# Kernel optimization log

Measured on AMD Instinct MI355X. Metric: run time of the kernel, lower is better.

The kernel has to match this reference:

```python
import jax, jax.numpy as jnp
import numpy as np

B, S, D, H, E, K = 4, 512, 1024, 16, 4, 2
HD = D // H
LN_EPS = 1e-5


def setup_inputs() -> dict:
    key = jax.random.key(0)
    ks = jax.random.split(key, 16)
    def w(k, shape, fan_in):
        return jax.random.normal(k, shape, jnp.float32) / np.float32(np.sqrt(fan_in))
    return {
        "x": jax.random.normal(ks[0], (B, S, D), jnp.float32),
        # stacked per-expert attention params [E, D, D] / [E, D]
        "Wq": w(ks[1], (E, D, D), D), "bq": jnp.zeros((E, D), jnp.float32),
        "Wk": w(ks[2], (E, D, D), D), "bk": jnp.zeros((E, D), jnp.float32),
        "Wv": w(ks[3], (E, D, D), D), "bv": jnp.zeros((E, D), jnp.float32),
        "Wo": w(ks[4], (E, D, D), D), "bo": jnp.zeros((E, D), jnp.float32),
        # router: Linear(D->D/2), LayerNorm, relu, Linear(D/2->E)
        "Wr1": w(ks[5], (D, D // 2), D), "br1": jnp.zeros((D // 2,), jnp.float32),
        "ln_g": jnp.ones((D // 2,), jnp.float32), "ln_b": jnp.zeros((D // 2,), jnp.float32),
        "Wr2": w(ks[6], (D // 2, E), D // 2), "br2": jnp.zeros((E,), jnp.float32),
    }


def _moe_attention(x, Wq, bq, Wk, bk, Wv, bv, Wo, bo, Wr1, br1, ln_g, ln_b, Wr2, br2):
    # ---- router ----
    h = x @ Wr1 + br1                                        # [B,S,D/2]
    mu = jnp.mean(h, axis=-1, keepdims=True)
    var = jnp.var(h, axis=-1, keepdims=True)
    h = (h - mu) * jax.lax.rsqrt(var + LN_EPS) * ln_g + ln_b
    h = jax.nn.relu(h)
    logits = h @ Wr2 + br2                                   # [B,S,E]
    probs = jax.nn.softmax(logits, axis=-1)
    top_p, top_i = jax.lax.top_k(probs, K)                   # [B,S,K]
    # scatter-add of top-k probs into dense expert mask [B,S,E]
    emask = jnp.sum(jax.nn.one_hot(top_i, E, dtype=x.dtype) * top_p[..., None], axis=2)

    # ---- dense per-expert attention (naive: every expert on every token) ----
    def heads(t):  # [E,B,S,D] -> [E,B,H,S,HD]
        return t.reshape(E, B, S, H, HD).transpose(0, 1, 3, 2, 4)

    q = heads(jnp.einsum('bsd,edf->ebsf', x, Wq) + bq[:, None, None, :])
    k = heads(jnp.einsum('bsd,edf->ebsf', x, Wk) + bk[:, None, None, :])
    v = heads(jnp.einsum('bsd,edf->ebsf', x, Wv) + bv[:, None, None, :])

    scores = jnp.einsum('ebhqd,ebhkd->ebhqk', q, k) / np.float32(np.sqrt(HD))
    attn = jax.nn.softmax(scores, axis=-1)                   # [E,B,H,S,S]
    o = jnp.einsum('ebhqk,ebhkd->ebhqd', attn, v)
    o = o.transpose(0, 1, 3, 2, 4).reshape(E, B, S, D)
    o = jnp.einsum('ebsd,edf->ebsf', o, Wo) + bo[:, None, None, :]  # [E,B,S,D]

    # ---- masked combine ----
    return jnp.einsum('ebsd,bse->bsd', o, emask)


def reference(x, Wq, bq, Wk, bk, Wv, bv, Wo, bo, Wr1, br1, ln_g, ln_b, Wr2, br2):
    return _moe_attention(x, Wq, bq, Wk, bk, Wv, bv, Wo, bo,
                          Wr1, br1, ln_g, ln_b, Wr2, br2)
```

## Files before the change

kernel.cpp:

```cpp
#include <hip/hip_runtime.h>
#include <hip/hip_bf16.h>
#include <math.h>

#define B_   4
#define S_   512
#define D_   1024
#define H_   16
#define E_   4
#define HD_  64
#define D2_  512
#define NTOK (B_*S_)

#define TDE ((size_t)NTOK * D_)
#define WWE ((size_t)D_ * D_)
#define ND2 ((size_t)NTOK * D2_)

typedef unsigned short ushort;
typedef short shortv8 __attribute__((ext_vector_type(8)));
typedef ushort ushortv4 __attribute__((ext_vector_type(4)));
typedef _Float16 halfv8 __attribute__((ext_vector_type(8)));
typedef _Float16 halfv4 __attribute__((ext_vector_type(4)));
typedef float floatv4 __attribute__((ext_vector_type(4)));

__device__ __forceinline__ ushort f2bf(float f) {
    union { __hip_bfloat16 b; ushort u; } cv;
    cv.b = __float2bfloat16(f);
    return cv.u;
}
__device__ __forceinline__ float bf2f(ushort u) {
    union { ushort u; __hip_bfloat16 b; } cv;
    cv.u = u;
    return __bfloat162float(cv.b);
}
__device__ __forceinline__ void gload16(const void* g, void* l) {
    __builtin_amdgcn_global_load_lds(
        (const __attribute__((address_space(1))) unsigned int*)g,
        (__attribute__((address_space(3))) unsigned int*)l, 16, 0, 0);
}

__device__ __forceinline__ void gemm_core_bf(
    const ushort* __restrict__ A0, const ushort* __restrict__ A1,
    const ushort* __restrict__ B0, const ushort* __restrict__ B1,
    int K, int klen, int brow, int bcol, ushort* lds, floatv4 acc[4][4])
{
    const int tid  = threadIdx.x;
    const int wave = tid >> 6, lane = tid & 63;
    const int wm = wave >> 1, wn = wave & 1;
    const int lr = lane & 15, lc = lane >> 4;

    const ushort* gsrc[4] = {A0, A1, B0, B1};
    size_t goff[4][2];
    int    loff[4][2];
#pragma unroll
    for (int t = 0; t < 4; t++) {
#pragma unroll
        for (int s = 0; s < 2; s++) {
            int p = s * 256 + tid;
            int m = p >> 2;
            int c = (p & 3) ^ ((m >> 1) & 3);
            int r = (t < 2) ? (brow + m) : (bcol + m);
            goff[t][s] = (size_t)r * K + c * 8;
            loff[t][s] = t * 4096 + p * 8;
        }
    }

    int aoff[4], boff[4];
#pragma unroll
    for (int i = 0; i < 4; i++) {
        int ra = wm * 64 + i * 16 + lr;
        aoff[i] = ra * 32 + ((lc ^ ((ra >> 1) & 3)) * 8);
        int rb2 = wn * 64 + i * 16 + lr;
        boff[i] = rb2 * 32 + ((lc ^ ((rb2 >> 1) & 3)) * 8);
    }

#define STAGEB_(buf, kk) \
    _Pragma("unroll") for (int t = 0; t < 4; t++) \
    _Pragma("unroll") for (int s = 0; s < 2; s++) \
        gload16(gsrc[t] + goff[t][s] + (kk), lds + (buf) * 16384 + loff[t][s]);

    STAGEB_(0, 0)

    int cur = 0;
    for (int k0 = 0; k0 < klen; k0 += 32, cur ^= 1) {
        if (k0 + 32 < klen) {
            STAGEB_(cur ^ 1, k0 + 32)
            asm volatile("s_waitcnt vmcnt(8)" ::: "memory");
        } else {
            asm volatile("s_waitcnt vmcnt(0)" ::: "memory");
        }
        __builtin_amdgcn_s_barrier();
        __builtin_amdgcn_sched_barrier(0);

        const ushort* L = lds + cur * 16384;
        shortv8 ah[4], al[4], bh[4], bl[4];
#pragma unroll
        for (int i = 0; i < 4; i++) {
            ah[i] = *(const shortv8*)(L +         aoff[i]);
            al[i] = *(const shortv8*)(L +  4096 + aoff[i]);
            bh[i] = *(const shortv8*)(L +  8192 + boff[i]);
            bl[i] = *(const shortv8*)(L + 12288 + boff[i]);
        }
#pragma unroll
        for (int mi = 0; mi < 4; mi++)
#pragma unroll
            for (int nj = 0; nj < 4; nj++) {
                acc[mi][nj] = __builtin_amdgcn_mfma_f32_16x16x32_bf16(ah[mi], bh[nj], acc[mi][nj], 0, 0, 0);
                acc[mi][nj] = __builtin_amdgcn_mfma_f32_16x16x32_bf16(ah[mi], bl[nj], acc[mi][nj], 0, 0, 0);
                acc[mi][nj] = __builtin_amdgcn_mfma_f32_16x16x32_bf16(al[mi], bh[nj], acc[mi][nj], 0, 0, 0);
            }

        asm volatile("s_waitcnt lgkmcnt(0)" ::: "memory");
        __builtin_amdgcn_sched_barrier(0);
        __builtin_amdgcn_s_barrier();
    }
#undef STAGEB_
}

template<bool GATHER>
__device__ __forceinline__ void gemm_core_h1(
    const _Float16* __restrict__ A0, const _Float16* __restrict__ B0,
    const int* __restrict__ arow,
    int K, int klen, int brow, int bcol, _Float16* lds, floatv4 acc[4][4])
{
    const int tid  = threadIdx.x;
    const int wave = tid >> 6, lane = tid & 63;
    const int wm = wave >> 1, wn = wave & 1;
    const int lr = lane & 15, lc = lane >> 4;

    const _Float16* gsrc[2] = {A0, B0};
    size_t goff[2][2];
    int    loff[2][2];
#pragma unroll
    for (int t = 0; t < 2; t++) {
#pragma unroll
        for (int s = 0; s < 2; s++) {
            int p = s * 256 + tid;
            int m = p >> 2;
            int c = (p & 3) ^ ((m >> 1) & 3);
            int r;
            if (t == 0) r = GATHER ? (arow[m] & 0x7FFFFFFF) : (brow + m);
            else        r = bcol + m;
            goff[t][s] = (size_t)r * K + c * 8;
            loff[t][s] = t * 4096 + p * 8;
        }
    }

    int aoff[4], boff[4];
#pragma unroll
    for (int i = 0; i < 4; i++) {
        int ra = wm * 64 + i * 16 + lr;
        aoff[i] = ra * 32 + ((lc ^ ((ra >> 1) & 3)) * 8);
        int rb2 = wn * 64 + i * 16 + lr;
        boff[i] = rb2 * 32 + ((lc ^ ((rb2 >> 1) & 3)) * 8);
    }

#define STAGEH_(buf, kk) \
    _Pragma("unroll") for (int t = 0; t < 2; t++) \
    _Pragma("unroll") for (int s = 0; s < 2; s++) \
        gload16(gsrc[t] + goff[t][s] + (kk), lds + (buf) * 8192 + loff[t][s]);

    STAGEH_(0, 0)

    int cur = 0;
    for (int k0 = 0; k0 < klen; k0 += 32, cur ^= 1) {
        if (k0 + 32 < klen) {
            STAGEH_(cur ^ 1, k0 + 32)
            asm volatile("s_waitcnt vmcnt(4)" ::: "memory");
        } else {
            asm volatile("s_waitcnt vmcnt(0)" ::: "memory");
        }
        __builtin_amdgcn_s_barrier();
        __builtin_amdgcn_sched_barrier(0);

        const _Float16* L = lds + cur * 8192;
        halfv8 aa[4], bb[4];
#pragma unroll
        for (int i = 0; i < 4; i++) {
            aa[i] = *(const halfv8*)(L +        aoff[i]);
            bb[i] = *(const halfv8*)(L + 4096 + boff[i]);
        }
#pragma unroll
        for (int mi = 0; mi < 4; mi++)
#pragma unroll
            for (int nj = 0; nj < 4; nj++)
                acc[mi][nj] = __builtin_amdgcn_mfma_f32_16x16x32_f16(aa[mi], bb[nj], acc[mi][nj], 0, 0, 0);

        asm volatile("s_waitcnt lgkmcnt(0)" ::: "memory");
        __builtin_amdgcn_sched_barrier(0);
        __builtin_amdgcn_s_barrier();
    }
#undef STAGEH_
}

#define ACC_INIT(acc) \
    _Pragma("unroll") for (int i = 0; i < 4; i++) \
    _Pragma("unroll") for (int j = 0; j < 4; j++) \
    _Pragma("unroll") for (int q = 0; q < 4; q++) acc[i][j][q] = 0.f;

#define EPI_VARS \
    const int lane = threadIdx.x & 63, wave = threadIdx.x >> 6; \
    const int wm = wave >> 1, wn = wave & 1, lr = lane & 15, lc = lane >> 4;

__global__ __launch_bounds__(256, 2) void gemm_router(
    const ushort* __restrict__ xh, const ushort* __restrict__ xl,
    const ushort* __restrict__ wr1h, const ushort* __restrict__ wr1l,
    float* __restrict__ hpart)
{
    __shared__ ushort lds[32768];
    floatv4 acc[4][4];
    ACC_INIT(acc)

    const int lid = blockIdx.x + 4 * (blockIdx.y + 16 * blockIdx.z);
    const int nid = (lid & 7) * 32 + (lid >> 3);
    const int kz = nid >> 6;
    const int rem = nid & 63;
    const int brow = (rem >> 2) * 128, bcol = (rem & 3) * 128;

    const int koff = kz * 256;
    gemm_core_bf(xh + koff, xl + koff, wr1h + koff, wr1l + koff,
                 D_, 256, brow, bcol, lds, acc);

    float* C = hpart + (size_t)kz * ND2;
    EPI_VARS
#pragma unroll
    for (int mi = 0; mi < 4; mi++)
#pragma unroll
        for (int nj = 0; nj < 4; nj++)
#pragma unroll
            for (int i = 0; i < 4; i++) {
                int row = brow + wm * 64 + mi * 16 + lc * 4 + i;
                int col = bcol + wn * 64 + nj * 16 + lr;
                C[(size_t)row * D2_ + col] = acc[mi][nj][i];
            }
}

__global__ __launch_bounds__(256, 2) void gemm_proj(
    const _Float16* __restrict__ xf,
    const _Float16* __restrict__ wth,
    const float* __restrict__ bq, const float* __restrict__ bk, const float* __restrict__ bv,
    const int* __restrict__ idx, const int* __restrict__ meta,
    _Float16* __restrict__ qf, _Float16* __restrict__ kf, _Float16* __restrict__ vf)
{
    __shared__ _Float16 lds[16384];
    const int lid = blockIdx.x + 8 * (blockIdx.y + 16 * blockIdx.z);
    const int nid = (lid & 7) * 192 + (lid >> 3);
    const int z = nid >> 7;
    const int rem = nid & 127;
    const int brow = (rem >> 3) * 128, bcol = (rem & 7) * 128;

    if (z < 8) {
        const int slot = z >> 1, m = z & 1;
        const size_t so = (size_t)slot * TDE;
        const _Float16* Bm = wth + (size_t)(slot * 4 + 1 + m) * WWE;
        const float* bias = ((m == 0) ? bk : bv) + (size_t)slot * D_;
        _Float16* Oo = ((m == 0) ? kf : vf) + so;

        floatv4 acc[4][4];
        ACC_INIT(acc)
        gemm_core_h1<false>(xf, Bm, nullptr, D_, D_, brow, bcol, lds, acc);

        EPI_VARS
#pragma unroll
        for (int mi = 0; mi < 4; mi++)
#pragma unroll
            for (int nj = 0; nj < 4; nj++)
#pragma unroll
                for (int i = 0; i < 4; i++) {
                    int row = brow + wm * 64 + mi * 16 + lc * 4 + i;
                    int col = bcol + wn * 64 + nj * 16 + lr;
                    Oo[(size_t)row * D_ + col] = (_Float16)(acc[mi][nj][i] + bias[col]);
                }
    } else {
        const int e = z - 8;
        const int pcnt = meta[32 + e];
        if (brow >= pcnt) return;
        const int* arow = idx + e * 2048 + brow;
        const _Float16* Bm = wth + (size_t)(e * 4 + 0) * WWE;
        const float* bias = bq + (size_t)e * D_;
        const size_t so = (size_t)e * TDE;

        floatv4 acc[4][4];
        ACC_INIT(acc)
        gemm_core_h1<true>(xf, Bm, arow, D_, D_, brow, bcol, lds, acc);

        EPI_VARS
#pragma unroll
        for (int mi = 0; mi < 4; mi++)
#pragma unroll
            for (int nj = 0; nj < 4; nj++)
#pragma unroll
                for (int i = 0; i < 4; i++) {
                    int row = brow + wm * 64 + mi * 16 + lc * 4 + i;
                    int col = bcol + wn * 64 + nj * 16 + lr;
                    qf[so + (size_t)row * D_ + col] =
                        (_Float16)((acc[mi][nj][i] + bias[col]) * 0.125f);
                }
    }
}

__global__ __launch_bounds__(256, 2) void gemm_combine4(
    const _Float16* __restrict__ oh,
    const _Float16* __restrict__ wth,
    const float* __restrict__ bo, const float* __restrict__ emask,
    const int* __restrict__ idx, const int* __restrict__ meta,
    float* __restrict__ out4)
{
    __shared__ _Float16 lds[16384];
    const int lid = blockIdx.x + 8 * (blockIdx.y + 16 * blockIdx.z);
    const int nid = (lid & 7) * 64 + (lid >> 3);
    const int e = nid >> 7;
    const int rem = nid & 127;
    const int brow = (rem >> 3) * 128, bcol = (rem & 7) * 128;

    const int pcnt = meta[32 + e];
    if (brow >= pcnt) return;
    const size_t so = (size_t)e * TDE;
    const _Float16* Bm = wth + (size_t)(e * 4 + 3) * WWE;
    const float* bias = bo + (size_t)e * D_;
    const int* idxe = idx + e * 2048;

    floatv4 acc[4][4];
    ACC_INIT(acc)
    gemm_core_h1<false>(oh + so, Bm, nullptr, D_, D_, brow, bcol, lds, acc);

    float* dst = out4 + so;
    EPI_VARS
#pragma unroll
    for (int mi = 0; mi < 4; mi++)
#pragma unroll
        for (int nj = 0; nj < 4; nj++)
#pragma unroll
            for (int i = 0; i < 4; i++) {
                int srow = brow + wm * 64 + mi * 16 + lc * 4 + i;
                int raw = idxe[srow];
                if (raw >= 0) {
                    float s = emask[(size_t)raw * E_ + e];
                    int col = bcol + wn * 64 + nj * 16 + lr;
                    dst[(size_t)raw * D_ + col] = s * (acc[mi][nj][i] + bias[col]);
                }
            }
}

__global__ __launch_bounds__(256) void reduce_out(
    const float* __restrict__ out4, float* __restrict__ out)
{
    size_t i = (size_t)blockIdx.x * 256 + threadIdx.x;
    const float4* p = (const float4*)out4;
    float4 a = p[i], b = p[i + TDE / 4], c = p[i + 2 * (TDE / 4)], d = p[i + 3 * (TDE / 4)];
    float4 r;
    r.x = a.x + b.x + c.x + d.x;
    r.y = a.y + b.y + c.y + d.y;
    r.z = a.z + b.z + c.z + d.z;
    r.w = a.w + b.w + c.w + d.w;
    ((float4*)out)[i] = r;
}

__global__ __launch_bounds__(256) void build_lists(
    const float* __restrict__ emask, int* __restrict__ idx, int* __restrict__ meta)
{
    const int e = blockIdx.x;
    const int tid = threadIdx.x;
    __shared__ int scan[256];
    __shared__ int runsh;
    if (tid == 0) runsh = 0;
    int* idxe = idx + e * 2048;

    for (int b = 0; b < B_; b++) {
        __syncthreads();
        const int base = runsh;
        int t0 = b * 512 + tid * 2;
        int f0 = (emask[(size_t)t0 * E_ + e] != 0.f) ? 1 : 0;
        int f1 = (emask[(size_t)(t0 + 1) * E_ + e] != 0.f) ? 1 : 0;
        int my = f0 + f1;
        scan[tid] = my;
        __syncthreads();
        for (int off = 1; off < 256; off <<= 1) {
            int v = (tid >= off) ? scan[tid - off] : 0;
            __syncthreads();
            scan[tid] += v;
            __syncthreads();
        }
        int excl = scan[tid] - my;
        int cnt = scan[255];
        if (f0) idxe[base + excl] = t0;
        if (f1) idxe[base + excl + f0] = t0 + 1;
        int plen = (cnt + 63) & ~63;
        for (int i = cnt + tid; i < plen; i += 256)
            idxe[base + i] = (b * 512) | (int)0x80000000;
        if (tid == 0) {
            meta[e * 4 + b] = base;
            meta[16 + e * 4 + b] = plen >> 6;
            runsh = base + plen;
        }
    }
    __syncthreads();
    int total = runsh;
    if (tid == 0) meta[32 + e] = total;
    for (int i = total + tid; i < 2048; i += 256)
        idxe[i] = (int)0x80000000;
}

__global__ __launch_bounds__(256, 2) void attn_all(
    const _Float16* __restrict__ qf_, const _Float16* __restrict__ kf_,
    const _Float16* __restrict__ vf_,
    _Float16* __restrict__ oh_,
    const int* __restrict__ meta)
{
    const int lid = blockIdx.x + 8 * (blockIdx.y + 64 * blockIdx.z);
    const int nid = (lid & 7) * 256 + (lid >> 3);
    const int e = nid >> 9;
    const int rem = nid & 511;
    const int bhid = rem >> 3, qtile = rem & 7;
    const int bb = bhid >> 4, hh = bhid & 15;

    const int ptiles = meta[16 + e * 4 + bb];
    if (qtile >= ptiles) return;
    const int pstart = meta[e * 4 + bb];

    __shared__ _Float16 Kf[4096];
    __shared__ _Float16 Vt[64 * 72];
    __shared__ _Float16 Pw[4][16 * 72];

    const size_t zo = (size_t)e * TDE;
    const int tid = threadIdx.x;
    const int wave = tid >> 6, lane = tid & 63;
    const int lr = lane & 15, lc = lane >> 4;
    const int q0 = pstart + qtile * 64;
    const size_t kvbase = zo + (size_t)bb * S_ * D_ + hh * 64;
    const size_t qobase = zo + hh * 64;

    halfv8 qq[2];
    {
        size_t qoff = qobase + (size_t)(q0 + wave * 16 + lr) * D_ + lc * 8;
        qq[0] = *(const halfv8*)(qf_ + qoff);
        qq[1] = *(const halfv8*)(qf_ + qoff + 32);
    }

    floatv4 ov[4];
    float m4[4], l4[4];
#pragma unroll
    for (int df = 0; df < 4; df++)
#pragma unroll
        for (int i = 0; i < 4; i++) ov[df][i] = 0.f;
#pragma unroll
    for (int i = 0; i < 4; i++) { m4[i] = -3.0e38f; l4[i] = 0.f; }

    for (int kt = 0; kt < S_ / 64; kt++) {
        const int kk0 = kt * 64;
        __syncthreads();

#pragma unroll
        for (int s = 0; s < 2; s++) {
            int p = s * 256 + tid;
            int r = p >> 3;
            int c = (p & 7) ^ (r & 7);
            gload16(kf_ + kvbase + (size_t)(kk0 + r) * D_ + c * 8, Kf + p * 8);
        }
        {
            const _Float16* vsrc = vf_ + kvbase + (size_t)(kk0 + lane) * D_ + wave * 16;
            halfv8 v0 = *(const halfv8*)vsrc;
            halfv8 v1 = *(const halfv8*)(vsrc + 8);
#pragma unroll
            for (int j = 0; j < 8; j++) Vt[(wave * 16 + j) * 72 + lane] = v0[j];
#pragma unroll
            for (int j = 0; j < 8; j++) Vt[(wave * 16 + 8 + j) * 72 + lane] = v1[j];
        }
        __syncthreads();

        floatv4 sc[4];
#pragma unroll
        for (int n = 0; n < 4; n++)
#pragma unroll
            for (int i = 0; i < 4; i++) sc[n][i] = 0.f;
#pragma unroll
        for (int n = 0; n < 4; n++)
#pragma unroll
            for (int ds = 0; ds < 2; ds++) {
                int off = (16 * n + lr) * 64 + (((ds * 4 + lc) ^ (lr & 7)) * 8);
                halfv8 kr = *(const halfv8*)(Kf + off);
                sc[n] = __builtin_amdgcn_mfma_f32_16x16x32_f16(qq[ds], kr, sc[n], 0, 0, 0);
            }

        float tm[4];
#pragma unroll
        for (int i = 0; i < 4; i++)
            tm[i] = fmaxf(fmaxf(sc[0][i], sc[1][i]), fmaxf(sc[2][i], sc[3][i]));
#pragma unroll
        for (int off = 1; off <= 8; off <<= 1)
#pragma unroll
            for (int i = 0; i < 4; i++)
                tm[i] = fmaxf(tm[i], __shfl_xor(tm[i], off));

        float nm[4], sca[4], ps[4];
#pragma unroll
        for (int i = 0; i < 4; i++) {
            nm[i] = fmaxf(m4[i], tm[i]);
            sca[i] = __expf(m4[i] - nm[i]);
            ps[i] = 0.f;
        }
        float pval[4][4];
#pragma unroll
        for (int n = 0; n < 4; n++)
#pragma unroll
            for (int i = 0; i < 4; i++) {
                float p = __expf(sc[n][i] - nm[i]);
                pval[n][i] = p;
                ps[i] += p;
            }
#pragma unroll
        for (int off = 1; off <= 8; off <<= 1)
#pragma unroll
            for (int i = 0; i < 4; i++)
                ps[i] += __shfl_xor(ps[i], off);
#pragma unroll
        for (int i = 0; i < 4; i++) {
            l4[i] = l4[i] * sca[i] + ps[i];
            m4[i] = nm[i];
        }
#pragma unroll
        for (int df = 0; df < 4; df++)
#pragma unroll
            for (int i = 0; i < 4; i++) ov[df][i] *= sca[i];

#pragma unroll
        for (int n = 0; n < 4; n++)
#pragma unroll
            for (int i = 0; i < 4; i++)
                Pw[wave][(lc * 4 + i) * 72 + 16 * n + lr] = (_Float16)pval[n][i];
        __syncthreads();

#pragma unroll
        for (int ks = 0; ks < 2; ks++) {
            halfv8 pa = *(const halfv8*)(&Pw[wave][lr * 72 + ks * 32 + lc * 8]);
#pragma unroll
            for (int df = 0; df < 4; df++) {
                halfv8 vr = *(const halfv8*)(Vt + (df * 16 + lr) * 72 + ks * 32 + lc * 8);
                ov[df] = __builtin_amdgcn_mfma_f32_16x16x32_f16(pa, vr, ov[df], 0, 0, 0);
            }
        }
    }

#pragma unroll
    for (int df = 0; df < 4; df++)
#pragma unroll
        for (int i = 0; i < 4; i++) {
            float val = ov[df][i] / l4[i];
            size_t off = qobase + (size_t)(q0 + wave * 16 + lc * 4 + i) * D_ + df * 16 + lr;
            oh_[off] = (_Float16)val;
        }
}

__global__ __launch_bounds__(256) void split_f32(
    const float* __restrict__ in, ushort* __restrict__ hb, ushort* __restrict__ lb,
    _Float16* __restrict__ hf)
{
    int i = blockIdx.x * 256 + threadIdx.x;
    float4 v = ((const float4*)in)[i];
    float vv[4] = {v.x, v.y, v.z, v.w};
    ushortv4 hv, lv;
    halfv4 hhv;
#pragma unroll
    for (int j = 0; j < 4; j++) {
        ushort h = f2bf(vv[j]);
        hv[j] = h;
        lv[j] = f2bf(vv[j] - bf2f(h));
        hhv[j] = (_Float16)vv[j];
    }
    ((ushortv4*)hb)[i] = hv;
    ((ushortv4*)lb)[i] = lv;
    ((halfv4*)hf)[i] = hhv;
}

__global__ __launch_bounds__(256) void tsplit(
    const float* __restrict__ W, ushort* __restrict__ Th, ushort* __restrict__ Tl,
    int K, int N)
{
    __shared__ float tile[64][65];
    const int n0 = blockIdx.x * 64, k0 = blockIdx.y * 64;
    const int tid = threadIdx.x;
#pragma unroll
    for (int i = 0; i < 16; i++) {
        int idx = i * 256 + tid;
        int r = idx >> 6, c = idx & 63;
        tile[r][c] = W[(size_t)(k0 + r) * N + n0 + c];
    }
    __syncthreads();
#pragma unroll
    for (int i = 0; i < 16; i++) {
        int idx = i * 256 + tid;
        int rn = idx >> 6, ck = idx & 63;
        float v = tile[ck][rn];
        ushort h = f2bf(v);
        Th[(size_t)(n0 + rn) * K + k0 + ck] = h;
        Tl[(size_t)(n0 + rn) * K + k0 + ck] = f2bf(v - bf2f(h));
    }
}

__global__ __launch_bounds__(256) void tsplit16h(
    const float* __restrict__ Wq, const float* __restrict__ Wk,
    const float* __restrict__ Wv, const float* __restrict__ Wo,
    _Float16* __restrict__ Th)
{
    __shared__ float tile[64][65];
    const int mg = blockIdx.z;
    const int e = mg >> 2, m = mg & 3;
    const float* W = ((m == 0) ? Wq : (m == 1) ? Wk : (m == 2) ? Wv : Wo) + (size_t)e * WWE;
    _Float16* T = Th + (size_t)mg * WWE;
    const int n0 = blockIdx.x * 64, k0 = blockIdx.y * 64;
    const int tid = threadIdx.x;
#pragma unroll
    for (int i = 0; i < 16; i++) {
        int idx = i * 256 + tid;
        int r = idx >> 6, c = idx & 63;
        tile[r][c] = W[(size_t)(k0 + r) * D_ + n0 + c];
    }
    __syncthreads();
#pragma unroll
    for (int i = 0; i < 16; i++) {
        int idx = i * 256 + tid;
        int rn = idx >> 6, ck = idx & 63;
        T[(size_t)(n0 + rn) * D_ + k0 + ck] = (_Float16)tile[ck][rn];
    }
}

__global__ __launch_bounds__(256) void router_post(
    const float* __restrict__ hpart, const float* __restrict__ br1,
    const float* __restrict__ ln_g, const float* __restrict__ ln_b,
    const float* __restrict__ Wr2, const float* __restrict__ br2,
    float* __restrict__ emask)
{
    const int t = blockIdx.x;
    const int tid = threadIdx.x;
    __shared__ float red[256];
    __shared__ float logits[E_];

    const float* hp = hpart + (size_t)t * D2_;
    float x0 = hp[tid] + hp[ND2 + tid] + hp[2 * ND2 + tid] + hp[3 * ND2 + tid] + br1[tid];
    float x1 = hp[tid + 256] + hp[ND2 + tid + 256] + hp[2 * ND2 + tid + 256]
             + hp[3 * ND2 + tid + 256] + br1[tid + 256];

    red[tid] = x0 + x1; __syncthreads();
    for (int off = 128; off; off >>= 1) { if (tid < off) red[tid] += red[tid + off]; __syncthreads(); }
    float mu = red[0] * (1.f / 512.f);
    __syncthreads();

    float d0 = x0 - mu, d1 = x1 - mu;
    red[tid] = d0 * d0 + d1 * d1; __syncthreads();
    for (int off = 128; off; off >>= 1) { if (tid < off) red[tid] += red[tid + off]; __syncthreads(); }
    float rs = rsqrtf(red[0] * (1.f / 512.f) + 1e-5f);
    __syncthreads();

    float n0 = fmaxf(fmaf(d0 * rs, ln_g[tid],       ln_b[tid]),       0.f);
    float n1 = fmaxf(fmaf(d1 * rs, ln_g[tid + 256], ln_b[tid + 256]), 0.f);

    for (int e = 0; e < E_; e++) {
        red[tid] = n0 * Wr2[(size_t)tid * E_ + e] + n1 * Wr2[(size_t)(tid + 256) * E_ + e];
        __syncthreads();
        for (int off = 128; off; off >>= 1) { if (tid < off) red[tid] += red[tid + off]; __syncthreads(); }
        if (tid == 0) logits[e] = red[0] + br2[e];
        __syncthreads();
    }

    if (tid == 0) {
        float mx = fmaxf(fmaxf(logits[0], logits[1]), fmaxf(logits[2], logits[3]));
        float p[E_], sum = 0.f;
        for (int e = 0; e < E_; e++) { p[e] = expf(logits[e] - mx); sum += p[e]; }
        float inv = 1.f / sum;
        for (int e = 0; e < E_; e++) p[e] *= inv;
        int i1 = 0;
        for (int e = 1; e < E_; e++) if (p[e] > p[i1]) i1 = e;
        int i2 = -1;
        for (int e = 0; e < E_; e++) { if (e == i1) continue; if (i2 < 0 || p[e] > p[i2]) i2 = e; }
        float o[E_] = {0.f, 0.f, 0.f, 0.f};
        o[i1] = p[i1]; o[i2] = p[i2];
        for (int e = 0; e < E_; e++) emask[(size_t)t * E_ + e] = o[e];
    }
}

extern "C" void kernel_launch(void* const* d_in, const int* in_sizes, int n_in,
                              void* d_out, int out_size, void* d_ws, size_t ws_size,
                              hipStream_t stream) {
    const float* x   = (const float*)d_in[0];
    const float* Wq  = (const float*)d_in[1];
    const float* bq  = (const float*)d_in[2];
    const float* Wk  = (const float*)d_in[3];
    const float* bk  = (const float*)d_in[4];
    const float* Wv  = (const float*)d_in[5];
    const float* bv  = (const float*)d_in[6];
    const float* Wo  = (const float*)d_in[7];
    const float* bo  = (const float*)d_in[8];
    const float* Wr1 = (const float*)d_in[9];
    const float* br1 = (const float*)d_in[10];
    const float* lng = (const float*)d_in[11];
    const float* lnb = (const float*)d_in[12];
    const float* Wr2 = (const float*)d_in[13];
    const float* br2 = (const float*)d_in[14];

    float* out = (float*)d_out;
    char* w = (char*)d_ws;
    dim3 blk(256);
    const size_t MB = 1024ull * 1024ull;

    float*    emask = (float*)w;
    int*      idx   = (int*)(w + 64 * 1024);
    int*      meta  = (int*)(w + 96 * 1024);
    _Float16* wth   = (_Float16*)(w + 1 * MB);
    ushort*   wr1h  = (ushort*)(w + 33 * MB);
    ushort*   wr1l  = (ushort*)(w + 34 * MB);
    ushort*   xh    = (ushort*)(w + 35 * MB);
    ushort*   xl    = (ushort*)(w + 39 * MB);
    _Float16* xfh   = (_Float16*)(w + 43 * MB);
    float*    hpart = (float*)(w + 47 * MB);
    _Float16* qfb   = (_Float16*)(w + 63 * MB);
    _Float16* kfb   = (_Float16*)(w + 79 * MB);
    _Float16* vfb   = (_Float16*)(w + 95 * MB);
    _Float16* ohb   = (_Float16*)(w + 111 * MB);
    float*    out4  = (float*)(w + 127 * MB);

    split_f32<<<dim3(NTOK * D_ / 1024), blk, 0, stream>>>(x, xh, xl, xfh);
    tsplit<<<dim3(D2_ / 64, D_ / 64), blk, 0, stream>>>(Wr1, wr1h, wr1l, D_, D2_);
    tsplit16h<<<dim3(16, 16, 16), blk, 0, stream>>>(Wq, Wk, Wv, Wo, wth);

    gemm_router<<<dim3(D2_ / 128, NTOK / 128, 4), blk, 0, stream>>>(
        xh, xl, wr1h, wr1l, hpart);
    router_post<<<dim3(NTOK), blk, 0, stream>>>(hpart, br1, lng, lnb, Wr2, br2, emask);
    build_lists<<<dim3(E_), blk, 0, stream>>>(emask, idx, meta);

    gemm_proj<<<dim3(D_ / 128, NTOK / 128, 12), blk, 0, stream>>>(
        xfh, wth, bq, bk, bv, idx, meta, qfb, kfb, vfb);

    attn_all<<<dim3(S_ / 64, B_ * H_, E_), blk, 0, stream>>>(
        qfb, kfb, vfb, ohb, meta);

    hipMemsetAsync(out4, 0, 4 * TDE * sizeof(float), stream);
    gemm_combine4<<<dim3(D_ / 128, NTOK / 128, 4), blk, 0, stream>>>(
        ohb, wth, bo, emask, idx, meta, out4);
    reduce_out<<<dim3(TDE / 1024), blk, 0, stream>>>(out4, out);
}
```

Measured before the change: 222.5 us.

## Use two rank slots for combine output and drop memset; raise occupancy bounds

Each token goes to exactly two experts, so build_lists now tags each entry with a rank bit (whether an earlier expert also selected the token). The combine GEMM then writes into one of two dense output slabs instead of four. This removes the 32MB memset of the four-slab buffer and halves the reduce kernel's reads, since every token lands in both slabs. The GEMM and attention kernels also raise their launch_bounds min-blocks hint, which may force register spills. Correctness relies on every token having exactly two nonzero mask entries; a zero top-k probability would leave a slab slot unwritten.

```diff
diff --git a/kernel.cpp b/kernel.cpp
--- a/kernel.cpp
+++ b/kernel.cpp
@@ -138,7 +138,7 @@
             int m = p >> 2;
             int c = (p & 3) ^ ((m >> 1) & 3);
             int r;
-            if (t == 0) r = GATHER ? (arow[m] & 0x7FFFFFFF) : (brow + m);
+            if (t == 0) r = GATHER ? (arow[m] & 0xFFFF) : (brow + m);
             else        r = bcol + m;
             goff[t][s] = (size_t)r * K + c * 8;
             loff[t][s] = t * 4096 + p * 8;
@@ -201,7 +201,7 @@
     const int lane = threadIdx.x & 63, wave = threadIdx.x >> 6; \
     const int wm = wave >> 1, wn = wave & 1, lr = lane & 15, lc = lane >> 4;
 
-__global__ __launch_bounds__(256, 2) void gemm_router(
+__global__ __launch_bounds__(256, 4) void gemm_router(
     const ushort* __restrict__ xh, const ushort* __restrict__ xl,
     const ushort* __restrict__ wr1h, const ushort* __restrict__ wr1l,
     float* __restrict__ hpart)
@@ -234,7 +234,7 @@
             }
 }
 
-__global__ __launch_bounds__(256, 2) void gemm_proj(
+__global__ __launch_bounds__(256, 4) void gemm_proj(
     const _Float16* __restrict__ xf,
     const _Float16* __restrict__ wth,
     const float* __restrict__ bq, const float* __restrict__ bk, const float* __restrict__ bv,
@@ -298,12 +298,12 @@
     }
 }
 
-__global__ __launch_bounds__(256, 2) void gemm_combine4(
+__global__ __launch_bounds__(256, 4) void gemm_combine4(
     const _Float16* __restrict__ oh,
     const _Float16* __restrict__ wth,
     const float* __restrict__ bo, const float* __restrict__ emask,
     const int* __restrict__ idx, const int* __restrict__ meta,
-    float* __restrict__ out4)
+    float* __restrict__ out2)
 {
     __shared__ _Float16 lds[16384];
     const int lid = blockIdx.x + 8 * (blockIdx.y + 16 * blockIdx.z);
@@ -323,7 +323,6 @@
     ACC_INIT(acc)
     gemm_core_h1<false>(oh + so, Bm, nullptr, D_, D_, brow, bcol, lds, acc);
 
-    float* dst = out4 + so;
     EPI_VARS
 #pragma unroll
     for (int mi = 0; mi < 4; mi++)
@@ -334,24 +333,27 @@
                 int srow = brow + wm * 64 + mi * 16 + lc * 4 + i;
                 int raw = idxe[srow];
                 if (raw >= 0) {
-                    float s = emask[(size_t)raw * E_ + e];
+                    int row = raw & 0xFFFF;
+                    int rank = (raw >> 30) & 1;
+                    float s = emask[(size_t)row * E_ + e];
                     int col = bcol + wn * 64 + nj * 16 + lr;
-                    dst[(size_t)raw * D_ + col] = s * (acc[mi][nj][i] + bias[col]);
+                    out2[(size_t)rank * TDE + (size_t)row * D_ + col] =
+                        s * (acc[mi][nj][i] + bias[col]);
                 }
             }
 }
 
 __global__ __launch_bounds__(256) void reduce_out(
-    const float* __restrict__ out4, float* __restrict__ out)
+    const float* __restrict__ out2, float* __restrict__ out)
 {
     size_t i = (size_t)blockIdx.x * 256 + threadIdx.x;
-    const float4* p = (const float4*)out4;
-    float4 a = p[i], b = p[i + TDE / 4], c = p[i + 2 * (TDE / 4)], d = p[i + 3 * (TDE / 4)];
+    const float4* p = (const float4*)out2;
+    float4 a = p[i], b = p[i + TDE / 4];
     float4 r;
-    r.x = a.x + b.x + c.x + d.x;
-    r.y = a.y + b.y + c.y + d.y;
-    r.z = a.z + b.z + c.z + d.z;
-    r.w = a.w + b.w + c.w + d.w;
+    r.x = a.x + b.x;
+    r.y = a.y + b.y;
+    r.z = a.z + b.z;
+    r.w = a.w + b.w;
     ((float4*)out)[i] = r;
 }
 
@@ -382,8 +384,18 @@
         }
         int excl = scan[tid] - my;
         int cnt = scan[255];
-        if (f0) idxe[base + excl] = t0;
-        if (f1) idxe[base + excl + f0] = t0 + 1;
+        if (f0) {
+            int rank = 0;
+            for (int ep = 0; ep < e; ep++)
+                if (emask[(size_t)t0 * E_ + ep] != 0.f) rank = 1;
+            idxe[base + excl] = t0 | (rank << 30);
+        }
+        if (f1) {
+            int rank = 0;
+            for (int ep = 0; ep < e; ep++)
+                if (emask[(size_t)(t0 + 1) * E_ + ep] != 0.f) rank = 1;
+            idxe[base + excl + f0] = (t0 + 1) | (rank << 30);
+        }
         int plen = (cnt + 63) & ~63;
         for (int i = cnt + tid; i < plen; i += 256)
             idxe[base + i] = (b * 512) | (int)0x80000000;
@@ -400,7 +412,7 @@
         idxe[i] = (int)0x80000000;
 }
 
-__global__ __launch_bounds__(256, 2) void attn_all(
+__global__ __launch_bounds__(256, 3) void attn_all(
     const _Float16* __restrict__ qf_, const _Float16* __restrict__ kf_,
     const _Float16* __restrict__ vf_,
     _Float16* __restrict__ oh_,
@@ -715,7 +727,7 @@
     _Float16* kfb   = (_Float16*)(w + 79 * MB);
     _Float16* vfb   = (_Float16*)(w + 95 * MB);
     _Float16* ohb   = (_Float16*)(w + 111 * MB);
-    float*    out4  = (float*)(w + 127 * MB);
+    float*    out2  = (float*)(w + 127 * MB);
 
     split_f32<<<dim3(NTOK * D_ / 1024), blk, 0, stream>>>(x, xh, xl, xfh);
     tsplit<<<dim3(D2_ / 64, D_ / 64), blk, 0, stream>>>(Wr1, wr1h, wr1l, D_, D2_);
@@ -732,8 +744,7 @@
     attn_all<<<dim3(S_ / 64, B_ * H_, E_), blk, 0, stream>>>(
         qfb, kfb, vfb, ohb, meta);
 
-    hipMemsetAsync(out4, 0, 4 * TDE * sizeof(float), stream);
     gemm_combine4<<<dim3(D_ / 128, NTOK / 128, 4), blk, 0, stream>>>(
-        ohb, wth, bo, emask, idx, meta, out4);
-    reduce_out<<<dim3(TDE / 1024), blk, 0, stream>>>(out4, out);
-}
+        ohb, wth, bo, emask, idx, meta, out2);
+    reduce_out<<<dim3(TDE / 1024), blk, 0, stream>>>(out2, out);
+}
```

Result: faster. 215.4 us (-3.2%).
